# Kernel tuning notes

Hardware: AMD Instinct MI355X
Metric: run time of the kernel (lower is better)

## Reference

```python
import jax, jax.numpy as jnp
import numpy as np

N = 50000   # nodes
E = 800000  # edges
F = 64      # input features
H = 64      # hidden (nhid)
C = 10      # classes
G = 500     # graphs in batch


def setup_inputs() -> dict:
    key = jax.random.key(0)
    ks = jax.random.split(key, 12)
    s = lambda fan: np.float32(1.0 / np.sqrt(fan))
    return {
        "x": jax.random.normal(ks[0], (N, F), jnp.float32),
        "edge_index": jax.random.randint(ks[1], (2, E), 0, N, dtype=jnp.int64),
        "batch": jnp.sort(jax.random.randint(ks[2], (N,), 0, G, dtype=jnp.int64)),
        "W1": jax.random.normal(ks[3], (F, H), jnp.float32) * s(F),
        "b1": jnp.zeros((H,), jnp.float32),
        "W2": jax.random.normal(ks[4], (H, H), jnp.float32) * s(H),
        "b2": jnp.zeros((H,), jnp.float32),
        "W3": jax.random.normal(ks[5], (H, H), jnp.float32) * s(H),
        "b3": jnp.zeros((H,), jnp.float32),
        "lin1_W": jax.random.normal(ks[6], (H, H), jnp.float32) * s(H),
        "lin1_b": jnp.zeros((H,), jnp.float32),
        "lin2_W": jax.random.normal(ks[7], (H, C), jnp.float32) * s(H),
        "lin2_b": jnp.zeros((C,), jnp.float32),
    }


def reference(x, edge_index, batch, W1, b1, W2, b2, W3, b3, lin1_W, lin1_b, lin2_W, lin2_b):
    n = x.shape[0]
    loops = jnp.arange(n, dtype=edge_index.dtype)
    src = jnp.concatenate([edge_index[0], loops])  # message sources (x_j)
    dst = jnp.concatenate([edge_index[1], loops])  # aggregation targets
    # symmetric GCN normalization on A + I
    deg = jax.ops.segment_sum(jnp.ones(src.shape, x.dtype), dst, num_segments=n)
    dis = jax.lax.rsqrt(deg)  # deg >= 1 thanks to self-loops
    norm = (dis[src] * dis[dst])[:, None]  # [E+N, 1]

    def gcn_relu(h, W, b):
        h = h @ W                                   # [N, H]
        agg = jax.ops.segment_sum(h[src] * norm, dst, num_segments=n)
        return jax.nn.relu(agg + b)

    h = gcn_relu(x, W1, b1)
    h = gcn_relu(h, W2, b2)
    h = gcn_relu(h, W3, b3)

    # global mean pool per graph
    sums = jax.ops.segment_sum(h, batch, num_segments=G)
    counts = jax.ops.segment_sum(jnp.ones((n,), h.dtype), batch, num_segments=G)
    pooled = sums / jnp.maximum(counts, 1.0)[:, None]  # [G, H]

    h = jax.nn.relu(pooled @ lin1_W + lin1_b)
    # dropout is identity in eval mode
    logits = h @ lin2_W + lin2_b
    return jax.nn.log_softmax(logits, axis=-1)
```

## Files before the change

kernel.cpp:

```cpp
#include <hip/hip_runtime.h>

#define NN 50000
#define NE 800000
#define HD 64
#define NC 10
#define NG 500
#define CAP 64
#define NBLK 196
#define NPART 8
#define PSZ 6250
#define FILLB 2048
#define MBLK 782

typedef float f32x4 __attribute__((ext_vector_type(4)));
typedef short bf16x8 __attribute__((ext_vector_type(8)));

__device__ __forceinline__ float bf16_to_f32(unsigned short h) {
    union { unsigned int u; float f; } v;
    v.u = ((unsigned int)h) << 16;
    return v.f;
}
__device__ __forceinline__ unsigned short f32_to_bf16(float f) {
    union { float f; unsigned int u; } v;
    v.f = f;
    unsigned int r = v.u + 0x7FFFu + ((v.u >> 16) & 1u);
    return (unsigned short)(r >> 16);
}

__device__ __forceinline__ void load_wfrags(const float* __restrict__ W, int lane,
                                            bf16x8 bh[4][2], bf16x8 bl[4][2]) {
    int col = lane & 15, krow = (lane >> 4) * 8;
#pragma unroll
    for (int n = 0; n < 4; ++n)
#pragma unroll
        for (int kt = 0; kt < 2; ++kt)
#pragma unroll
            for (int j = 0; j < 8; ++j) {
                float wv = W[(kt * 32 + krow + j) * 64 + n * 16 + col];
                unsigned short h = f32_to_bf16(wv);
                float rem = wv - bf16_to_f32(h);
                bh[n][kt][j] = (short)h;
                bl[n][kt][j] = (short)f32_to_bf16(rem);
            }
}

__global__ void init_k(int* __restrict__ rowcnt) {
    int i = blockIdx.x * 256 + threadIdx.x;
    if (i < NN) rowcnt[i] = 0;
}

__global__ __launch_bounds__(256) void fill3_k(
    const int* __restrict__ src, const int* __restrict__ dst,
    int* __restrict__ rowcnt, unsigned short* __restrict__ col16) {
    int part = blockIdx.x & (NPART - 1);
    int blk = blockIdx.x >> 3;
    int dlo = part * PSZ, dhi = dlo + PSZ;
    int stride = (FILLB / NPART) * 256;
    for (int e = blk * 256 + threadIdx.x; e < NE; e += stride) {
        int d = dst[e];
        if (d >= dlo && d < dhi) {
            int p = atomicAdd(&rowcnt[d], 1);
            if (p < CAP) col16[(size_t)d * CAP + p] = (unsigned short)src[e];
        }
    }
}

__global__ __launch_bounds__(256) void mfma_gemm1_k(
    const float* __restrict__ x, const float* __restrict__ W,
    const int* __restrict__ rowcnt, unsigned short* __restrict__ out16) {
    __shared__ unsigned short A[64][72];
    int t = threadIdx.x, lane = t & 63, w = t >> 6;
    int base = blockIdx.x * 64;
#pragma unroll
    for (int i = 0; i < 4; ++i) {
        int idx = t + i * 256;
        int row = idx >> 4, c4 = (idx & 15) * 4;
        int r = base + row;
        float4 v = make_float4(0.f, 0.f, 0.f, 0.f);
        if (r < NN) v = ((const float4*)x)[(size_t)r * 16 + (idx & 15)];
        unsigned int p0 = f32_to_bf16(v.x) | ((unsigned int)f32_to_bf16(v.y) << 16);
        unsigned int p1 = f32_to_bf16(v.z) | ((unsigned int)f32_to_bf16(v.w) << 16);
        *(unsigned int*)&A[row][c4] = p0;
        *(unsigned int*)&A[row][c4 + 2] = p1;
    }
    bf16x8 bh[4][2], bl[4][2];
    load_wfrags(W, lane, bh, bl);
    __syncthreads();
    int col = lane & 15, krow = (lane >> 4) * 8;
    bf16x8 a0 = *(const bf16x8*)&A[w * 16 + col][krow];
    bf16x8 a1 = *(const bf16x8*)&A[w * 16 + col][32 + krow];
    f32x4 acc[4];
#pragma unroll
    for (int n = 0; n < 4; ++n) { acc[n] = (f32x4){0.f, 0.f, 0.f, 0.f}; }
#pragma unroll
    for (int n = 0; n < 4; ++n) {
        acc[n] = __builtin_amdgcn_mfma_f32_16x16x32_bf16(a0, bh[n][0], acc[n], 0, 0, 0);
        acc[n] = __builtin_amdgcn_mfma_f32_16x16x32_bf16(a1, bh[n][1], acc[n], 0, 0, 0);
        acc[n] = __builtin_amdgcn_mfma_f32_16x16x32_bf16(a0, bl[n][0], acc[n], 0, 0, 0);
        acc[n] = __builtin_amdgcn_mfma_f32_16x16x32_bf16(a1, bl[n][1], acc[n], 0, 0, 0);
    }
    int row0 = base + w * 16 + (lane >> 4) * 4;
    float di[4];
#pragma unroll
    for (int r = 0; r < 4; ++r)
        di[r] = (row0 + r < NN) ? rsqrtf((float)(rowcnt[row0 + r] + 1)) : 1.f;
#pragma unroll
    for (int n = 0; n < 4; ++n)
#pragma unroll
        for (int r = 0; r < 4; ++r) {
            int row = row0 + r;
            if (row < NN)
                out16[(size_t)row * HD + n * 16 + col] = f32_to_bf16(acc[n][r] * di[r]);
        }
}

__global__ __launch_bounds__(256) void agg_mfma_k(
    const unsigned short* __restrict__ tin, const int* __restrict__ rowcnt,
    const unsigned short* __restrict__ col16, const float* __restrict__ bias,
    const float* __restrict__ W, unsigned short* __restrict__ tout) {
    __shared__ unsigned short A[64][72];
    __shared__ float dibuf[64];
    int t = threadIdx.x, lane = t & 63, w = t >> 6;
    int base = blockIdx.x * 64;
    float bv = bias[lane];
    for (int n16 = 0; n16 < 16; ++n16) {
        int wid = base + w * 16 + n16;
        float r = 0.f, di = 1.f;
        if (wid < NN) {
            int colv = col16[(size_t)wid * CAP + lane];
            int c0 = rowcnt[wid];
            di = rsqrtf((float)(c0 + 1));
            int cnt = c0 > CAP ? CAP : c0;
            float acc[8];
#pragma unroll
            for (int j = 0; j < 8; ++j) acc[j] = 0.f;
            acc[0] = bf16_to_f32(tin[(size_t)wid * HD + lane]);
            int e = 0;
            for (; e + 7 < cnt; e += 8) {
#pragma unroll
                for (int j = 0; j < 8; ++j) {
                    int s = __shfl(colv, e + j);
                    acc[j] += bf16_to_f32(tin[(size_t)s * HD + lane]);
                }
            }
            for (; e < cnt; ++e) {
                int s = __shfl(colv, e);
                acc[0] += bf16_to_f32(tin[(size_t)s * HD + lane]);
            }
            float s01 = (acc[0] + acc[1]) + (acc[2] + acc[3]);
            float s23 = (acc[4] + acc[5]) + (acc[6] + acc[7]);
            r = fmaxf((s01 + s23) * di + bv, 0.f);
        }
        A[w * 16 + n16][lane] = f32_to_bf16(r);
        if (lane == 0) dibuf[w * 16 + n16] = di;
    }
    bf16x8 bh[4][2], bl[4][2];
    load_wfrags(W, lane, bh, bl);
    __syncthreads();
    int col = lane & 15, krow = (lane >> 4) * 8;
    bf16x8 a0 = *(const bf16x8*)&A[w * 16 + col][krow];
    bf16x8 a1 = *(const bf16x8*)&A[w * 16 + col][32 + krow];
    f32x4 acc[4];
#pragma unroll
    for (int n = 0; n < 4; ++n) { acc[n] = (f32x4){0.f, 0.f, 0.f, 0.f}; }
#pragma unroll
    for (int n = 0; n < 4; ++n) {
        acc[n] = __builtin_amdgcn_mfma_f32_16x16x32_bf16(a0, bh[n][0], acc[n], 0, 0, 0);
        acc[n] = __builtin_amdgcn_mfma_f32_16x16x32_bf16(a1, bh[n][1], acc[n], 0, 0, 0);
        acc[n] = __builtin_amdgcn_mfma_f32_16x16x32_bf16(a0, bl[n][0], acc[n], 0, 0, 0);
        acc[n] = __builtin_amdgcn_mfma_f32_16x16x32_bf16(a1, bl[n][1], acc[n], 0, 0, 0);
    }
    int row0 = base + w * 16 + (lane >> 4) * 4;
    float dr[4];
#pragma unroll
    for (int r = 0; r < 4; ++r) dr[r] = dibuf[w * 16 + (lane >> 4) * 4 + r];
#pragma unroll
    for (int n = 0; n < 4; ++n)
#pragma unroll
        for (int r = 0; r < 4; ++r) {
            int row = row0 + r;
            if (row < NN)
                tout[(size_t)row * HD + n * 16 + col] = f32_to_bf16(acc[n][r] * dr[r]);
        }
}

__global__ __launch_bounds__(256) void agg_k(
    const unsigned short* __restrict__ tin, const int* __restrict__ rowcnt,
    const unsigned short* __restrict__ col16, const float* __restrict__ bias,
    float* __restrict__ out) {
    int wid = blockIdx.x * 4 + (threadIdx.x >> 6);
    int lane = threadIdx.x & 63;
    if (wid >= NN) return;
    int colv = col16[(size_t)wid * CAP + lane];
    int c0 = rowcnt[wid];
    float di = rsqrtf((float)(c0 + 1));
    int cnt = c0 > CAP ? CAP : c0;
    float acc[8];
#pragma unroll
    for (int j = 0; j < 8; ++j) acc[j] = 0.f;
    acc[0] = bf16_to_f32(tin[(size_t)wid * HD + lane]);
    int e = 0;
    for (; e + 7 < cnt; e += 8) {
#pragma unroll
        for (int j = 0; j < 8; ++j) {
            int s = __shfl(colv, e + j);
            acc[j] += bf16_to_f32(tin[(size_t)s * HD + lane]);
        }
    }
    for (; e < cnt; ++e) {
        int s = __shfl(colv, e);
        acc[0] += bf16_to_f32(tin[(size_t)s * HD + lane]);
    }
    float s01 = (acc[0] + acc[1]) + (acc[2] + acc[3]);
    float s23 = (acc[4] + acc[5]) + (acc[6] + acc[7]);
    out[(size_t)wid * HD + lane] = fmaxf((s01 + s23) * di + bias[lane], 0.f);
}

__global__ __launch_bounds__(256) void poolhead_k(
    const float* __restrict__ h, const int* __restrict__ batch,
    const float* __restrict__ l1W, const float* __restrict__ l1b,
    const float* __restrict__ l2W, const float* __restrict__ l2b,
    float* __restrict__ out) {
    __shared__ float part[4][64];
    __shared__ float p[64];
    __shared__ float hsm[64];
    __shared__ float lg[NC];
    __shared__ int ss[2];
    int g = blockIdx.x;
    int t = threadIdx.x, lane = t & 63, w = t >> 6;
    if (t < 2) {
        int target = g + t;
        int lo = 0, hi = NN;
        while (lo < hi) {
            int mid = (lo + hi) >> 1;
            if (batch[mid] < target) lo = mid + 1; else hi = mid;
        }
        ss[t] = lo;
    }
    __syncthreads();
    int s0 = ss[0], s1 = ss[1];
    float acc = 0.f;
    for (int i = s0 + w; i < s1; i += 4) acc += h[(size_t)i * HD + lane];
    part[w][lane] = acc;
    __syncthreads();
    if (t < 64) {
        float s = part[0][t] + part[1][t] + part[2][t] + part[3][t];
        float c = (float)(s1 - s0);
        p[t] = s / fmaxf(c, 1.0f);
    }
    __syncthreads();
    if (t < 64) {
        float a = l1b[t];
#pragma unroll
        for (int k = 0; k < 64; ++k) a += p[k] * l1W[k * 64 + t];
        hsm[t] = fmaxf(a, 0.f);
    }
    __syncthreads();
    if (t < NC) {
        float a = l2b[t];
#pragma unroll
        for (int k = 0; k < 64; ++k) a += hsm[k] * l2W[k * NC + t];
        lg[t] = a;
    }
    __syncthreads();
    if (t < NC) {
        float m = -1e30f;
#pragma unroll
        for (int k = 0; k < NC; ++k) m = fmaxf(m, lg[k]);
        float s = 0.f;
#pragma unroll
        for (int k = 0; k < NC; ++k) s += expf(lg[k] - m);
        out[(size_t)g * NC + t] = lg[t] - m - logf(s);
    }
}

extern "C" void kernel_launch(void* const* d_in, const int* in_sizes, int n_in,
                              void* d_out, int out_size, void* d_ws, size_t ws_size,
                              hipStream_t stream) {
    const float* x = (const float*)d_in[0];
    const int* ei = (const int*)d_in[1];
    const int* src = ei;
    const int* dst = ei + NE;
    const int* batch = (const int*)d_in[2];
    const float* W1 = (const float*)d_in[3];
    const float* b1 = (const float*)d_in[4];
    const float* W2 = (const float*)d_in[5];
    const float* b2 = (const float*)d_in[6];
    const float* W3 = (const float*)d_in[7];
    const float* b3 = (const float*)d_in[8];
    const float* l1W = (const float*)d_in[9];
    const float* l1b = (const float*)d_in[10];
    const float* l2W = (const float*)d_in[11];
    const float* l2b = (const float*)d_in[12];
    float* out = (float*)d_out;

    char* p = (char*)d_ws;
    auto alloc = [&](size_t bytes) {
        char* r = p;
        p += (bytes + 255) & ~(size_t)255;
        return r;
    };
    int* rowcnt = (int*)alloc(NN * 4);
    unsigned short* col16 = (unsigned short*)alloc((size_t)NN * CAP * 2);
    unsigned short* tmpA = (unsigned short*)alloc((size_t)NN * HD * 2);
    unsigned short* tmpB = (unsigned short*)alloc((size_t)NN * HD * 2);
    float* hcur = (float*)alloc((size_t)NN * HD * 4);

    init_k<<<NBLK, 256, 0, stream>>>(rowcnt);
    fill3_k<<<FILLB, 256, 0, stream>>>(src, dst, rowcnt, col16);

    mfma_gemm1_k<<<MBLK, 256, 0, stream>>>(x, W1, rowcnt, tmpA);
    agg_mfma_k<<<MBLK, 256, 0, stream>>>(tmpA, rowcnt, col16, b1, W2, tmpB);
    agg_mfma_k<<<MBLK, 256, 0, stream>>>(tmpB, rowcnt, col16, b2, W3, tmpA);
    agg_k<<<(NN + 3) / 4, 256, 0, stream>>>(tmpA, rowcnt, col16, b3, hcur);

    poolhead_k<<<NG, 256, 0, stream>>>(hcur, batch, l1W, l1b, l2W, l2b, out);
}
```

Baseline: 272.3 us.

## Fuse final aggregation with mean-pool atomics and widen aggregate-GEMM blocks

The last GCN aggregation now adds its ReLU outputs directly into a per-graph pooled buffer using run-length partial sums and atomics. This removes the fp32 hidden-state write and the pooling kernel's re-read of it, and poolhead shrinks to a small MLP over the pooled sums. The fused aggregate-GEMM kernels move to 512 threads with 8 rows per wave, prefetch column indices and counts, and stage the split hi/lo bf16 weights in shared memory instead of per-wave registers. In exchange, atomic float adds make the pooled sums order-nondeterministic, and half the waves sit idle during the MFMA phase.

```diff
diff --git a/kernel.cpp b/kernel.cpp
--- a/kernel.cpp
+++ b/kernel.cpp
@@ -27,6 +27,31 @@
     return (unsigned short)(r >> 16);
 }
 
+__device__ __forceinline__ float gather_relu(
+    const unsigned short* __restrict__ tin, int wid, int colv, int c0,
+    float di, float bv, int lane) {
+    int cnt = c0 > CAP ? CAP : c0;
+    float acc[8];
+#pragma unroll
+    for (int j = 0; j < 8; ++j) acc[j] = 0.f;
+    acc[0] = bf16_to_f32(tin[(size_t)wid * HD + lane]);
+    int e = 0;
+    for (; e + 7 < cnt; e += 8) {
+#pragma unroll
+        for (int j = 0; j < 8; ++j) {
+            int s = __shfl(colv, e + j);
+            acc[j] += bf16_to_f32(tin[(size_t)s * HD + lane]);
+        }
+    }
+    for (; e < cnt; ++e) {
+        int s = __shfl(colv, e);
+        acc[0] += bf16_to_f32(tin[(size_t)s * HD + lane]);
+    }
+    float s01 = (acc[0] + acc[1]) + (acc[2] + acc[3]);
+    float s23 = (acc[4] + acc[5]) + (acc[6] + acc[7]);
+    return fmaxf((s01 + s23) * di + bv, 0.f);
+}
+
 __device__ __forceinline__ void load_wfrags(const float* __restrict__ W, int lane,
                                             bf16x8 bh[4][2], bf16x8 bl[4][2]) {
     int col = lane & 15, krow = (lane >> 4) * 8;
@@ -44,9 +69,10 @@
             }
 }
 
-__global__ void init_k(int* __restrict__ rowcnt) {
+__global__ void init_k(int* __restrict__ rowcnt, float* __restrict__ pooled) {
     int i = blockIdx.x * 256 + threadIdx.x;
     if (i < NN) rowcnt[i] = 0;
+    if (i < NG * HD) pooled[i] = 0.f;
 }
 
 __global__ __launch_bounds__(256) void fill3_k(
@@ -114,120 +140,120 @@
         }
 }
 
-__global__ __launch_bounds__(256) void agg_mfma_k(
+__global__ __launch_bounds__(512) void agg_mfma_k(
     const unsigned short* __restrict__ tin, const int* __restrict__ rowcnt,
     const unsigned short* __restrict__ col16, const float* __restrict__ bias,
     const float* __restrict__ W, unsigned short* __restrict__ tout) {
     __shared__ unsigned short A[64][72];
+    __shared__ unsigned short Whi[64][72];
+    __shared__ unsigned short Wlo[64][72];
     __shared__ float dibuf[64];
     int t = threadIdx.x, lane = t & 63, w = t >> 6;
     int base = blockIdx.x * 64;
     float bv = bias[lane];
-    for (int n16 = 0; n16 < 16; ++n16) {
-        int wid = base + w * 16 + n16;
+    int colv[8], c0[8];
+#pragma unroll
+    for (int n = 0; n < 8; ++n) {
+        int wid = base + w * 8 + n;
+        bool v = wid < NN;
+        colv[n] = v ? (int)col16[(size_t)wid * CAP + lane] : 0;
+        c0[n] = v ? rowcnt[wid] : -1;
+    }
+#pragma unroll
+    for (int i = 0; i < 8; ++i) {
+        int idx = t + i * 512;
+        int k = idx >> 6, c = idx & 63;
+        float wv = W[idx];
+        unsigned short h = f32_to_bf16(wv);
+        Whi[c][k] = h;
+        Wlo[c][k] = f32_to_bf16(wv - bf16_to_f32(h));
+    }
+#pragma unroll
+    for (int n = 0; n < 8; ++n) {
+        int row = w * 8 + n;
         float r = 0.f, di = 1.f;
-        if (wid < NN) {
-            int colv = col16[(size_t)wid * CAP + lane];
-            int c0 = rowcnt[wid];
-            di = rsqrtf((float)(c0 + 1));
-            int cnt = c0 > CAP ? CAP : c0;
-            float acc[8];
-#pragma unroll
-            for (int j = 0; j < 8; ++j) acc[j] = 0.f;
-            acc[0] = bf16_to_f32(tin[(size_t)wid * HD + lane]);
-            int e = 0;
-            for (; e + 7 < cnt; e += 8) {
-#pragma unroll
-                for (int j = 0; j < 8; ++j) {
-                    int s = __shfl(colv, e + j);
-                    acc[j] += bf16_to_f32(tin[(size_t)s * HD + lane]);
-                }
-            }
-            for (; e < cnt; ++e) {
-                int s = __shfl(colv, e);
-                acc[0] += bf16_to_f32(tin[(size_t)s * HD + lane]);
-            }
-            float s01 = (acc[0] + acc[1]) + (acc[2] + acc[3]);
-            float s23 = (acc[4] + acc[5]) + (acc[6] + acc[7]);
-            r = fmaxf((s01 + s23) * di + bv, 0.f);
-        }
-        A[w * 16 + n16][lane] = f32_to_bf16(r);
-        if (lane == 0) dibuf[w * 16 + n16] = di;
-    }
-    bf16x8 bh[4][2], bl[4][2];
-    load_wfrags(W, lane, bh, bl);
-    __syncthreads();
+        if (c0[n] >= 0) {
+            di = rsqrtf((float)(c0[n] + 1));
+            r = gather_relu(tin, base + row, colv[n], c0[n], di, bv, lane);
+        }
+        A[row][lane] = f32_to_bf16(r);
+        if (lane == 0) dibuf[row] = di;
+    }
+    __syncthreads();
+    if (w >= 4) return;
     int col = lane & 15, krow = (lane >> 4) * 8;
     bf16x8 a0 = *(const bf16x8*)&A[w * 16 + col][krow];
     bf16x8 a1 = *(const bf16x8*)&A[w * 16 + col][32 + krow];
-    f32x4 acc[4];
-#pragma unroll
-    for (int n = 0; n < 4; ++n) { acc[n] = (f32x4){0.f, 0.f, 0.f, 0.f}; }
+    float dr[4];
+#pragma unroll
+    for (int r = 0; r < 4; ++r) dr[r] = dibuf[w * 16 + (lane >> 4) * 4 + r];
+    int row0 = base + w * 16 + (lane >> 4) * 4;
 #pragma unroll
     for (int n = 0; n < 4; ++n) {
-        acc[n] = __builtin_amdgcn_mfma_f32_16x16x32_bf16(a0, bh[n][0], acc[n], 0, 0, 0);
-        acc[n] = __builtin_amdgcn_mfma_f32_16x16x32_bf16(a1, bh[n][1], acc[n], 0, 0, 0);
-        acc[n] = __builtin_amdgcn_mfma_f32_16x16x32_bf16(a0, bl[n][0], acc[n], 0, 0, 0);
-        acc[n] = __builtin_amdgcn_mfma_f32_16x16x32_bf16(a1, bl[n][1], acc[n], 0, 0, 0);
-    }
-    int row0 = base + w * 16 + (lane >> 4) * 4;
-    float dr[4];
-#pragma unroll
-    for (int r = 0; r < 4; ++r) dr[r] = dibuf[w * 16 + (lane >> 4) * 4 + r];
-#pragma unroll
-    for (int n = 0; n < 4; ++n)
+        bf16x8 bh0 = *(const bf16x8*)&Whi[n * 16 + col][krow];
+        bf16x8 bh1 = *(const bf16x8*)&Whi[n * 16 + col][32 + krow];
+        bf16x8 bl0 = *(const bf16x8*)&Wlo[n * 16 + col][krow];
+        bf16x8 bl1 = *(const bf16x8*)&Wlo[n * 16 + col][32 + krow];
+        f32x4 acc = (f32x4){0.f, 0.f, 0.f, 0.f};
+        acc = __builtin_amdgcn_mfma_f32_16x16x32_bf16(a0, bh0, acc, 0, 0, 0);
+        acc = __builtin_amdgcn_mfma_f32_16x16x32_bf16(a1, bh1, acc, 0, 0, 0);
+        acc = __builtin_amdgcn_mfma_f32_16x16x32_bf16(a0, bl0, acc, 0, 0, 0);
+        acc = __builtin_amdgcn_mfma_f32_16x16x32_bf16(a1, bl1, acc, 0, 0, 0);
 #pragma unroll
         for (int r = 0; r < 4; ++r) {
             int row = row0 + r;
             if (row < NN)
-                tout[(size_t)row * HD + n * 16 + col] = f32_to_bf16(acc[n][r] * dr[r]);
-        }
-}
-
-__global__ __launch_bounds__(256) void agg_k(
+                tout[(size_t)row * HD + n * 16 + col] = f32_to_bf16(acc[r] * dr[r]);
+        }
+    }
+}
+
+__global__ __launch_bounds__(512) void agg_pool_k(
     const unsigned short* __restrict__ tin, const int* __restrict__ rowcnt,
     const unsigned short* __restrict__ col16, const float* __restrict__ bias,
-    float* __restrict__ out) {
-    int wid = blockIdx.x * 4 + (threadIdx.x >> 6);
-    int lane = threadIdx.x & 63;
-    if (wid >= NN) return;
-    int colv = col16[(size_t)wid * CAP + lane];
-    int c0 = rowcnt[wid];
-    float di = rsqrtf((float)(c0 + 1));
-    int cnt = c0 > CAP ? CAP : c0;
-    float acc[8];
-#pragma unroll
-    for (int j = 0; j < 8; ++j) acc[j] = 0.f;
-    acc[0] = bf16_to_f32(tin[(size_t)wid * HD + lane]);
-    int e = 0;
-    for (; e + 7 < cnt; e += 8) {
-#pragma unroll
-        for (int j = 0; j < 8; ++j) {
-            int s = __shfl(colv, e + j);
-            acc[j] += bf16_to_f32(tin[(size_t)s * HD + lane]);
-        }
-    }
-    for (; e < cnt; ++e) {
-        int s = __shfl(colv, e);
-        acc[0] += bf16_to_f32(tin[(size_t)s * HD + lane]);
-    }
-    float s01 = (acc[0] + acc[1]) + (acc[2] + acc[3]);
-    float s23 = (acc[4] + acc[5]) + (acc[6] + acc[7]);
-    out[(size_t)wid * HD + lane] = fmaxf((s01 + s23) * di + bias[lane], 0.f);
-}
-
-__global__ __launch_bounds__(256) void poolhead_k(
-    const float* __restrict__ h, const int* __restrict__ batch,
+    const int* __restrict__ batch, float* __restrict__ pooled) {
+    int t = threadIdx.x, lane = t & 63, w = t >> 6;
+    int base = blockIdx.x * 64 + w * 8;
+    float bv = bias[lane];
+    int colv[8], c0[8];
+#pragma unroll
+    for (int n = 0; n < 8; ++n) {
+        int wid = base + n;
+        bool v = wid < NN;
+        colv[n] = v ? (int)col16[(size_t)wid * CAP + lane] : 0;
+        c0[n] = v ? rowcnt[wid] : -1;
+    }
+    int curg = -1;
+    float psum = 0.f;
+#pragma unroll
+    for (int n = 0; n < 8; ++n) {
+        if (c0[n] >= 0) {
+            int wid = base + n;
+            float di = rsqrtf((float)(c0[n] + 1));
+            float r = gather_relu(tin, wid, colv[n], c0[n], di, bv, lane);
+            int g = batch[wid];
+            if (g != curg) {
+                if (curg >= 0) atomicAdd(&pooled[(size_t)curg * HD + lane], psum);
+                curg = g;
+                psum = r;
+            } else {
+                psum += r;
+            }
+        }
+    }
+    if (curg >= 0) atomicAdd(&pooled[(size_t)curg * HD + lane], psum);
+}
+
+__global__ __launch_bounds__(64) void poolhead_k(
+    const float* __restrict__ pooled, const int* __restrict__ batch,
     const float* __restrict__ l1W, const float* __restrict__ l1b,
     const float* __restrict__ l2W, const float* __restrict__ l2b,
     float* __restrict__ out) {
-    __shared__ float part[4][64];
     __shared__ float p[64];
     __shared__ float hsm[64];
     __shared__ float lg[NC];
     __shared__ int ss[2];
-    int g = blockIdx.x;
-    int t = threadIdx.x, lane = t & 63, w = t >> 6;
+    int g = blockIdx.x, t = threadIdx.x;
     if (t < 2) {
         int target = g + t;
         int lo = 0, hi = NN;
@@ -238,29 +264,19 @@
         ss[t] = lo;
     }
     __syncthreads();
-    int s0 = ss[0], s1 = ss[1];
-    float acc = 0.f;
-    for (int i = s0 + w; i < s1; i += 4) acc += h[(size_t)i * HD + lane];
-    part[w][lane] = acc;
-    __syncthreads();
-    if (t < 64) {
-        float s = part[0][t] + part[1][t] + part[2][t] + part[3][t];
-        float c = (float)(s1 - s0);
-        p[t] = s / fmaxf(c, 1.0f);
-    }
-    __syncthreads();
-    if (t < 64) {
-        float a = l1b[t];
-#pragma unroll
-        for (int k = 0; k < 64; ++k) a += p[k] * l1W[k * 64 + t];
-        hsm[t] = fmaxf(a, 0.f);
-    }
+    float c = (float)(ss[1] - ss[0]);
+    p[t] = pooled[(size_t)g * HD + t] / fmaxf(c, 1.0f);
+    __syncthreads();
+    float a = l1b[t];
+#pragma unroll
+    for (int k = 0; k < 64; ++k) a += p[k] * l1W[k * 64 + t];
+    hsm[t] = fmaxf(a, 0.f);
     __syncthreads();
     if (t < NC) {
-        float a = l2b[t];
-#pragma unroll
-        for (int k = 0; k < 64; ++k) a += hsm[k] * l2W[k * NC + t];
-        lg[t] = a;
+        float a2 = l2b[t];
+#pragma unroll
+        for (int k = 0; k < 64; ++k) a2 += hsm[k] * l2W[k * NC + t];
+        lg[t] = a2;
     }
     __syncthreads();
     if (t < NC) {
@@ -304,15 +320,15 @@
     unsigned short* col16 = (unsigned short*)alloc((size_t)NN * CAP * 2);
     unsigned short* tmpA = (unsigned short*)alloc((size_t)NN * HD * 2);
     unsigned short* tmpB = (unsigned short*)alloc((size_t)NN * HD * 2);
-    float* hcur = (float*)alloc((size_t)NN * HD * 4);
-
-    init_k<<<NBLK, 256, 0, stream>>>(rowcnt);
+    float* pooled = (float*)alloc((size_t)NG * HD * 4);
+
+    init_k<<<NBLK, 256, 0, stream>>>(rowcnt, pooled);
     fill3_k<<<FILLB, 256, 0, stream>>>(src, dst, rowcnt, col16);
 
     mfma_gemm1_k<<<MBLK, 256, 0, stream>>>(x, W1, rowcnt, tmpA);
-    agg_mfma_k<<<MBLK, 256, 0, stream>>>(tmpA, rowcnt, col16, b1, W2, tmpB);
-    agg_mfma_k<<<MBLK, 256, 0, stream>>>(tmpB, rowcnt, col16, b2, W3, tmpA);
-    agg_k<<<(NN + 3) / 4, 256, 0, stream>>>(tmpA, rowcnt, col16, b3, hcur);
-
-    poolhead_k<<<NG, 256, 0, stream>>>(hcur, batch, l1W, l1b, l2W, l2b, out);
-}
+    agg_mfma_k<<<MBLK, 512, 0, stream>>>(tmpA, rowcnt, col16, b1, W2, tmpB);
+    agg_mfma_k<<<MBLK, 512, 0, stream>>>(tmpB, rowcnt, col16, b2, W3, tmpA);
+    agg_pool_k<<<MBLK, 512, 0, stream>>>(tmpA, rowcnt, col16, b3, batch, pooled);
+
+    poolhead_k<<<NG, 64, 0, stream>>>(pooled, batch, l1W, l1b, l2W, l2b, out);
+}
```

Result: faster. 244.4 us (-10.2%).
